# Kernel tuning notes

Measured on AMD Instinct MI355X. Metric: run time of the kernel, lower is better.

## Reference

```python
import jax, jax.numpy as jnp
import numpy as np

POOLING_COUNTS = [15, 8, 8]
N = 128
D = 256
B = 16


def _build_specs():
    # Replicates the (kernel, stride, i, j) schedule of SparseConv.__init__.
    specs = []
    stride, offset = 1, 0
    for ci, c in enumerate(POOLING_COUNTS):
        for k in range(c):
            offset += stride
            i = np.arange(0, N - offset, stride)
            j = np.arange(offset, N, stride)
            kern = 3 if (ci > 0 and k == 0) else 2  # first conv of later groups downsamples
            st = 2 if (ci > 0 and k == 0) else 1
            specs.append((kern, st, i, j))
        stride *= 2
    return specs

SPECS = _build_specs()
N_K2 = sum(1 for s in SPECS if s[0] == 2)  # 29 kernel-2 stride-1 convs
N_K3 = sum(1 for s in SPECS if s[0] == 3)  # 2 kernel-3 stride-2 convs


def _conv1d(x, w, b, stride):
    # x: (B, D, L), w: (O, I, K) -> (B, O, L_out), VALID padding like nn.Conv1d
    y = jax.lax.conv_general_dilated(x, w, (stride,), 'VALID',
                                     dimension_numbers=('NCH', 'OIH', 'NCH'))
    return y + b[None, :, None]


def setup_inputs() -> dict:
    key = jax.random.key(0)
    ks = jax.random.split(key, 5)
    scale = 1.0 / np.sqrt(2.0 * D)  # ~ PyTorch Conv1d default init scale
    return {
        'x': jax.random.normal(ks[0], (B, D, N), jnp.float32),
        'w2': jax.random.normal(ks[1], (N_K2, D, D, 2), jnp.float32) * scale,
        'b2': jax.random.normal(ks[2], (N_K2, D), jnp.float32) * scale,
        'w3': jax.random.normal(ks[3], (N_K3, D, D, 3), jnp.float32) * scale,
        'b3': jax.random.normal(ks[4], (N_K3, D), jnp.float32) * scale,
    }


def reference(x, w2, b2, w3, b3):
    diag = np.arange(N)
    # map2d[:, :, i, i] = x
    map2d = jnp.zeros((B, D, N, N), x.dtype).at[:, :, diag, diag].set(x)
    c2 = c3 = 0
    for kern, st, i, j in SPECS:  # fixed-length chain of 31 structurally distinct convs
        if kern == 2:
            x = _conv1d(x, w2[c2], b2[c2], 1)
            c2 += 1
        else:
            x = _conv1d(x, w3[c3], b3[c3], 2)
            c3 += 1
        map2d = map2d.at[:, :, i, j].set(x)  # scatter stripe into sparse 2D map
    return map2d
```

## Files before the change

kernel.cpp:

```cpp
#include <hip/hip_runtime.h>

typedef __bf16 bf16x8 __attribute__((ext_vector_type(8)));
typedef float  floatx4 __attribute__((ext_vector_type(4)));
typedef float  fvec4  __attribute__((ext_vector_type(4)));
typedef unsigned short ushort4v __attribute__((ext_vector_type(4)));
typedef unsigned short ushort8v __attribute__((ext_vector_type(8)));

__device__ __forceinline__ unsigned short f2bf(float f) {
  unsigned int u = __float_as_uint(f);
  u = u + 0x7FFFu + ((u >> 16) & 1u);
  return (unsigned short)(u >> 16);
}

#define WP3_OFF   3801088
#define X0_OFF    4194304
#define Y_OFF_B   (64u << 20)

__global__ __launch_bounds__(256) void prep_kernel(
    const float* __restrict__ w2, const float* __restrict__ w3,
    const float* __restrict__ x, unsigned short* __restrict__ ws)
{
  int g = blockIdx.x * 256 + threadIdx.x;
  const float* src; unsigned short* dst;
  if (g < 950272)            { src = w2; dst = ws; }
  else if (g < 950272+98304) { g -= 950272; src = w3; dst = ws + WP3_OFF; }
  else                       { g -= (950272+98304); src = x; dst = ws + X0_OFF; }
  fvec4 v = *reinterpret_cast<const fvec4*>(src + 4*g);
  ushort4v o;
  o[0] = f2bf(v[0]); o[1] = f2bf(v[1]); o[2] = f2bf(v[2]); o[3] = f2bf(v[3]);
  *reinterpret_cast<ushort4v*>(dst + 4*g) = o;
}

template<int KW>
__global__ __launch_bounds__(256) void conv_kernel(
    const unsigned short* __restrict__ Xin,
    unsigned short* __restrict__ Xout,
    const unsigned short* __restrict__ WP,
    const float* __restrict__ bias,
    float* __restrict__ Yl,
    int Lin, int Lpin, int Lout, int Lpout)
{
  constexpr int CS   = (KW == 3) ? 2 : 1;
  constexpr int KS   = 256 * KW;
  constexpr int pitch = KS + 8;
  constexpr int NV   = (KW == 2) ? 5 : 9;
  __shared__ unsigned short LA[32 * pitch];

  const int tid = threadIdx.x;
  const int b   = blockIdx.z;
  const int m0  = blockIdx.x * 32;
  const int n0  = blockIdx.y * 64;

  {
    const int i = tid;
    const unsigned short* rp = Xin + ((b * 256 + i) * Lpin) + CS * m0;
    ushort8v xr[NV];
#pragma unroll
    for (int v = 0; v < NV; ++v)
      xr[v] = *reinterpret_cast<const ushort8v*>(rp + v * 8);
    const unsigned short* xs = reinterpret_cast<const unsigned short*>(xr);
    if (KW == 2) {
#pragma unroll
      for (int m = 0; m < 32; ++m) {
        unsigned int pk = (unsigned int)xs[m] | ((unsigned int)xs[m + 1] << 16);
        *reinterpret_cast<unsigned int*>(&LA[m * pitch + 2 * i]) = pk;
      }
    } else {
#pragma unroll
      for (int m = 0; m < 32; ++m) {
        int base = m * pitch + 3 * i;
        LA[base]     = xs[2 * m];
        LA[base + 1] = xs[2 * m + 1];
        LA[base + 2] = xs[2 * m + 2];
      }
    }
  }
  __syncthreads();

  const int wave = tid >> 6, lane = tid & 63;
  const int l15 = lane & 15, quad = lane >> 4;
  const int nn = n0 + wave * 16 + l15;
  const unsigned short* wrow = WP + (long)nn * KS;
  const int kbase = quad * 8;

  floatx4 acc0 = {0.f, 0.f, 0.f, 0.f};
  floatx4 acc1 = {0.f, 0.f, 0.f, 0.f};

  constexpr int niter = KS / 32;
#pragma unroll
  for (int kc = 0; kc < niter; ++kc) {
    int ko = kc * 32 + kbase;
    bf16x8 bfrag = *reinterpret_cast<const bf16x8*>(wrow + ko);
    bf16x8 a0 = *reinterpret_cast<const bf16x8*>(&LA[l15 * pitch + ko]);
    bf16x8 a1 = *reinterpret_cast<const bf16x8*>(&LA[(16 + l15) * pitch + ko]);
    acc0 = __builtin_amdgcn_mfma_f32_16x16x32_bf16(a0, bfrag, acc0, 0, 0, 0);
    acc1 = __builtin_amdgcn_mfma_f32_16x16x32_bf16(a1, bfrag, acc1, 0, 0, 0);
  }

  const float bv = bias[nn];
  const int row = b * 256 + nn;
  unsigned short* xo = Xout + row * Lpout;
  float* yo = Yl + row * 128;
#pragma unroll
  for (int r = 0; r < 4; ++r) {
    int m = m0 + quad * 4 + r;
    if (m < Lout) {
      float v = acc0[r] + bv;
      xo[m] = f2bf(v);
      yo[m] = v;
    }
    int m2 = m0 + 16 + quad * 4 + r;
    if (m2 < Lout) {
      float v = acc1[r] + bv;
      xo[m2] = f2bf(v);
      yo[m2] = v;
    }
  }
}

__global__ __launch_bounds__(256) void assemble_kernel(
    float* __restrict__ out, const float* __restrict__ x, const float* __restrict__ Y)
{
  __shared__ float S[32 * 129];
  const int blk = blockIdx.x;
  const int tid = threadIdx.x;

  {
    const int m = tid & 127, half = tid >> 7;
#pragma unroll
    for (int lp = 0; lp < 16; ++lp) {
      const int l = lp * 2 + half;
      if (l < 31) {
        const int Lout = (l < 15) ? (127 - l)
                       : (l == 15) ? 56
                       : (l < 23)  ? (71 - l)
                       : (l == 23) ? 24 : (47 - l);
        if (m < Lout) S[l * 129 + m] = Y[(long)l * 524288 + blk * 128 + m];
      } else {
        S[31 * 129 + m] = x[blk * 128 + m];
      }
    }
  }
  __syncthreads();

  const long obase = (long)blk << 14;
#pragma unroll 1
  for (int it = 0; it < 16; ++it) {
    const int flat = it * 256 + tid;
    const int r = flat >> 5, c0 = (flat & 31) << 2;
    fvec4 v = {0.f, 0.f, 0.f, 0.f};
#pragma unroll
    for (int jj = 0; jj < 4; ++jj) {
      const int d = c0 + jj - r;
      if (d == 0)                 v[jj] = S[31 * 129 + r];
      else if (d >= 1 && d <= 15) v[jj] = S[(d - 1) * 129 + r];
      else if (d >= 17 && d <= 31 && (d & 1) == 1 && (r & 1) == 0)
        v[jj] = S[(15 + ((d - 17) >> 1)) * 129 + (r >> 1)];
      else if (d >= 35 && d <= 63 && (d & 3) == 3 && (r & 3) == 0)
        v[jj] = S[(23 + ((d - 35) >> 2)) * 129 + (r >> 2)];
    }
    *reinterpret_cast<fvec4*>(out + obase + 4 * flat) = v;
  }
}

extern "C" void kernel_launch(void* const* d_in, const int* in_sizes, int n_in,
                              void* d_out, int out_size, void* d_ws, size_t ws_size,
                              hipStream_t stream)
{
  const float* x  = (const float*)d_in[0];
  const float* w2 = (const float*)d_in[1];
  const float* b2 = (const float*)d_in[2];
  const float* w3 = (const float*)d_in[3];
  const float* b3 = (const float*)d_in[4];
  float* out = (float*)d_out;
  unsigned short* ws = (unsigned short*)d_ws;
  float* Y = (float*)((char*)d_ws + Y_OFF_B);

  prep_kernel<<<4608, 256, 0, stream>>>(w2, w3, x, ws);

  const int counts[3] = {15, 8, 8};
  int stride = 1, offset = 0;
  int Lin = 128, Lpin = 128;
  int c2 = 0, c3 = 0, lidx = 0;
  long xprev = X0_OFF;
  long xnext = xprev + (long)16 * 256 * 128 + 64;
  for (int ci = 0; ci < 3; ++ci) {
    for (int k = 0; k < counts[ci]; ++k) {
      offset += stride;
      int KW = (ci > 0 && k == 0) ? 3 : 2;
      int cs = (KW == 3) ? 2 : 1;
      int Lout = (Lin - KW) / cs + 1;
      int Lpout = (Lout + 7) & ~7;
      const unsigned short* WPt; const float* bt;
      if (KW == 2) { WPt = ws + (long)c2 * 131072; bt = b2 + c2 * 256; ++c2; }
      else         { WPt = ws + WP3_OFF + (long)c3 * 196608; bt = b3 + c3 * 256; ++c3; }
      dim3 grid((Lout + 31) / 32, 4, 16);
      if (KW == 2)
        conv_kernel<2><<<grid, 256, 0, stream>>>(
            ws + xprev, ws + xnext, WPt, bt, Y + (long)lidx * 524288,
            Lin, Lpin, Lout, Lpout);
      else
        conv_kernel<3><<<grid, 256, 0, stream>>>(
            ws + xprev, ws + xnext, WPt, bt, Y + (long)lidx * 524288,
            Lin, Lpin, Lout, Lpout);
      ++lidx;
      xprev = xnext;
      xnext += (long)16 * 256 * Lpout + 64;
      Lin = Lout; Lpin = Lpout;
    }
    stride *= 2;
  }

  assemble_kernel<<<4096, 256, 0, stream>>>(out, x, Y);
}
```

Measured before the change: 540.8 us.

## Fuse chains of conv layers into group kernels with halo tiles in LDS

```diff
diff --git a/kernel.cpp b/kernel.cpp
--- a/kernel.cpp
+++ b/kernel.cpp
@@ -14,6 +14,7 @@
 
 #define WP3_OFF   3801088
 #define X0_OFF    4194304
+#define TBL_OFF_B (32u << 20)
 #define Y_OFF_B   (64u << 20)
 
 __global__ __launch_bounds__(256) void prep_kernel(
@@ -31,47 +32,66 @@
   *reinterpret_cast<ushort4v*>(dst + 4*g) = o;
 }
 
-template<int KW>
-__global__ __launch_bounds__(256) void conv_kernel(
+__global__ __launch_bounds__(256) void tbl_kernel(unsigned short* __restrict__ tbl)
+{
+  const int g = blockIdx.x * 256 + threadIdx.x;
+  const int r = g >> 7, c = g & 127, d = c - r;
+  unsigned short v = 0xFFFFu;
+  if (d == 0) v = (unsigned short)(31 * 129 + r);
+  else if (d >= 1 && d <= 15) v = (unsigned short)((d - 1) * 129 + r);
+  else if (d >= 17 && d <= 31 && (d & 1) == 1 && (r & 1) == 0)
+    v = (unsigned short)((15 + ((d - 17) >> 1)) * 129 + (r >> 1));
+  else if (d >= 35 && d <= 63 && (d & 3) == 3 && (r & 3) == 0)
+    v = (unsigned short)((23 + ((d - 35) >> 2)) * 129 + (r >> 2));
+  tbl[g] = v;
+}
+
+template<int NL, int KW0, int TW, int LPIN, int LOUT0, int LPOUT, bool XOUT>
+__global__ __launch_bounds__(512, 2) void fused_group(
     const unsigned short* __restrict__ Xin,
     unsigned short* __restrict__ Xout,
-    const unsigned short* __restrict__ WP,
-    const float* __restrict__ bias,
-    float* __restrict__ Yl,
-    int Lin, int Lpin, int Lout, int Lpout)
-{
-  constexpr int CS   = (KW == 3) ? 2 : 1;
-  constexpr int KS   = 256 * KW;
-  constexpr int pitch = KS + 8;
-  constexpr int NV   = (KW == 2) ? 5 : 9;
-  __shared__ unsigned short LA[32 * pitch];
+    const unsigned short* __restrict__ W2base,
+    const unsigned short* __restrict__ W3,
+    const float* __restrict__ B2base,
+    const float* __restrict__ B3,
+    float* __restrict__ Ybase)
+{
+  constexpr int K3   = (KW0 == 3) ? 1 : 0;
+  constexpr int W0   = TW + NL - 1;
+  constexpr int R0   = ((W0 + 15) / 16) * 16;
+  constexpr int R1   = ((W0 - 1 + 15) / 16) * 16;
+  constexpr int P0   = (KW0 == 3) ? 776 : 520;
+  constexpr int LDSA = P0 * R0;
+  constexpr int LDSB = 520 * R1;
+  __shared__ unsigned short LA[LDSA + LDSB];
 
   const int tid = threadIdx.x;
-  const int b   = blockIdx.z;
-  const int m0  = blockIdx.x * 32;
-  const int n0  = blockIdx.y * 64;
+  const int g = blockIdx.x, b = blockIdx.y;
+  const int t0 = g * TW;
 
   {
-    const int i = tid;
-    const unsigned short* rp = Xin + ((b * 256 + i) * Lpin) + CS * m0;
+    const int i = tid & 255, h = tid >> 8;
+    constexpr int SPAN = (KW0 == 3) ? (2 * W0 + 1) : (W0 + 1);
+    constexpr int NV = (SPAN + 7) / 8;
+    constexpr int HR = (W0 + 1) / 2;
+    const unsigned short* rp = Xin + (b * 256 + i) * LPIN + ((KW0 == 3) ? 2 * t0 : t0);
     ushort8v xr[NV];
 #pragma unroll
-    for (int v = 0; v < NV; ++v)
-      xr[v] = *reinterpret_cast<const ushort8v*>(rp + v * 8);
+    for (int v = 0; v < NV; ++v) xr[v] = *reinterpret_cast<const ushort8v*>(rp + v * 8);
     const unsigned short* xs = reinterpret_cast<const unsigned short*>(xr);
-    if (KW == 2) {
-#pragma unroll
-      for (int m = 0; m < 32; ++m) {
-        unsigned int pk = (unsigned int)xs[m] | ((unsigned int)xs[m + 1] << 16);
-        *reinterpret_cast<unsigned int*>(&LA[m * pitch + 2 * i]) = pk;
-      }
-    } else {
-#pragma unroll
-      for (int m = 0; m < 32; ++m) {
-        int base = m * pitch + 3 * i;
-        LA[base]     = xs[2 * m];
-        LA[base + 1] = xs[2 * m + 1];
-        LA[base + 2] = xs[2 * m + 2];
+#pragma unroll
+    for (int rr = 0; rr < HR; ++rr) {
+      const int r = h * HR + rr;
+      if (r < W0) {
+        if (KW0 == 2) {
+          unsigned int pk = (unsigned int)xs[r] | ((unsigned int)xs[r + 1] << 16);
+          *reinterpret_cast<unsigned int*>(&LA[r * 520 + 2 * i]) = pk;
+        } else {
+          const int base = r * 776 + 3 * i;
+          LA[base]     = xs[2 * r];
+          LA[base + 1] = xs[2 * r + 1];
+          LA[base + 2] = xs[2 * r + 2];
+        }
       }
     }
   }
@@ -79,47 +99,84 @@
 
   const int wave = tid >> 6, lane = tid & 63;
   const int l15 = lane & 15, quad = lane >> 4;
-  const int nn = n0 + wave * 16 + l15;
-  const unsigned short* wrow = WP + (long)nn * KS;
-  const int kbase = quad * 8;
-
-  floatx4 acc0 = {0.f, 0.f, 0.f, 0.f};
-  floatx4 acc1 = {0.f, 0.f, 0.f, 0.f};
-
-  constexpr int niter = KS / 32;
-#pragma unroll
-  for (int kc = 0; kc < niter; ++kc) {
-    int ko = kc * 32 + kbase;
-    bf16x8 bfrag = *reinterpret_cast<const bf16x8*>(wrow + ko);
-    bf16x8 a0 = *reinterpret_cast<const bf16x8*>(&LA[l15 * pitch + ko]);
-    bf16x8 a1 = *reinterpret_cast<const bf16x8*>(&LA[(16 + l15) * pitch + ko]);
-    acc0 = __builtin_amdgcn_mfma_f32_16x16x32_bf16(a0, bfrag, acc0, 0, 0, 0);
-    acc1 = __builtin_amdgcn_mfma_f32_16x16x32_bf16(a1, bfrag, acc1, 0, 0, 0);
-  }
-
-  const float bv = bias[nn];
-  const int row = b * 256 + nn;
-  unsigned short* xo = Xout + row * Lpout;
-  float* yo = Yl + row * 128;
-#pragma unroll
-  for (int r = 0; r < 4; ++r) {
-    int m = m0 + quad * 4 + r;
-    if (m < Lout) {
-      float v = acc0[r] + bv;
-      xo[m] = f2bf(v);
-      yo[m] = v;
-    }
-    int m2 = m0 + 16 + quad * 4 + r;
-    if (m2 < Lout) {
-      float v = acc1[r] + bv;
-      xo[m2] = f2bf(v);
-      yo[m2] = v;
-    }
+  const int nA = wave * 32 + l15, nB = nA + 16;
+
+#pragma unroll 1
+  for (int j = 0; j < NL; ++j) {
+    const int  Wj   = TW + NL - 1 - j;
+    const int  MTH  = (Wj + 15) >> 4;
+    const bool isK3 = (KW0 == 3) && (j == 0);
+    const int  K    = isK3 ? 768 : 512;
+    const int  NIT  = isK3 ? 24 : 16;
+    const int  pit  = isK3 ? 776 : 520;
+    const unsigned short* Wl = isK3 ? W3 : (W2base + (long)(j - K3) * 131072);
+    const float* bl = isK3 ? B3 : (B2base + (j - K3) * 256);
+    const unsigned short* src = LA + ((j & 1) ? LDSA : 0);
+    unsigned short*       dst = LA + ((j & 1) ? 0 : LDSA);
+
+    const unsigned short* wA = Wl + nA * K + quad * 8;
+    const unsigned short* wB = Wl + nB * K + quad * 8;
+    int ab[3];
+#pragma unroll
+    for (int t = 0; t < 3; ++t) ab[t] = (t * 16 + l15) * pit + quad * 8;
+
+    floatx4 acc[2][3];
+#pragma unroll
+    for (int p = 0; p < 2; ++p)
+#pragma unroll
+      for (int t = 0; t < 3; ++t) acc[p][t] = (floatx4){0.f, 0.f, 0.f, 0.f};
+
+#pragma unroll 4
+    for (int kc = 0; kc < NIT; ++kc) {
+      bf16x8 bA = *reinterpret_cast<const bf16x8*>(wA + kc * 32);
+      bf16x8 bB = *reinterpret_cast<const bf16x8*>(wB + kc * 32);
+#pragma unroll
+      for (int t = 0; t < 3; ++t) {
+        if (t < MTH) {
+          bf16x8 a = *reinterpret_cast<const bf16x8*>(&src[ab[t] + kc * 32]);
+          acc[0][t] = __builtin_amdgcn_mfma_f32_16x16x32_bf16(a, bA, acc[0][t], 0, 0, 0);
+          acc[1][t] = __builtin_amdgcn_mfma_f32_16x16x32_bf16(a, bB, acc[1][t], 0, 0, 0);
+        }
+      }
+    }
+
+    const float bvA = bl[nA], bvB = bl[nB];
+    const int Wn = Wj - 1;
+    const int Lout = LOUT0 - j;
+#pragma unroll
+    for (int p = 0; p < 2; ++p) {
+      const int n = p ? nB : nA;
+      const float bv = p ? bvB : bvA;
+      float* yr = Ybase + (long)j * 524288 + (b * 256 + n) * 128;
+      unsigned short* xo = XOUT ? (Xout + (b * 256 + n) * LPOUT) : (unsigned short*)0;
+#pragma unroll
+      for (int t = 0; t < 3; ++t) {
+        if (t < MTH) {
+#pragma unroll
+          for (int r = 0; r < 4; ++r) {
+            const int ro = t * 16 + quad * 4 + r;
+            const float v = acc[p][t][r] + bv;
+            const unsigned short bf = f2bf(v);
+            if (j < NL - 1) {
+              if (ro < Wn)            dst[ro * 520 + 2 * n]       = bf;
+              if (ro >= 1 && ro <= Wn) dst[(ro - 1) * 520 + 2 * n + 1] = bf;
+            }
+            const int m = t0 + ro;
+            if (ro < Wj && m < Lout) {
+              yr[m] = v;
+              if (XOUT && j == NL - 1) xo[m] = bf;
+            }
+          }
+        }
+      }
+    }
+    __syncthreads();
   }
 }
 
 __global__ __launch_bounds__(256) void assemble_kernel(
-    float* __restrict__ out, const float* __restrict__ x, const float* __restrict__ Y)
+    float* __restrict__ out, const float* __restrict__ x,
+    const unsigned short* __restrict__ tbl, const float* __restrict__ Y)
 {
   __shared__ float S[32 * 129];
   const int blk = blockIdx.x;
@@ -147,17 +204,14 @@
 #pragma unroll 1
   for (int it = 0; it < 16; ++it) {
     const int flat = it * 256 + tid;
-    const int r = flat >> 5, c0 = (flat & 31) << 2;
-    fvec4 v = {0.f, 0.f, 0.f, 0.f};
+    ushort4v t4 = *reinterpret_cast<const ushort4v*>(tbl + 4 * flat);
+    fvec4 v;
 #pragma unroll
     for (int jj = 0; jj < 4; ++jj) {
-      const int d = c0 + jj - r;
-      if (d == 0)                 v[jj] = S[31 * 129 + r];
-      else if (d >= 1 && d <= 15) v[jj] = S[(d - 1) * 129 + r];
-      else if (d >= 17 && d <= 31 && (d & 1) == 1 && (r & 1) == 0)
-        v[jj] = S[(15 + ((d - 17) >> 1)) * 129 + (r >> 1)];
-      else if (d >= 35 && d <= 63 && (d & 3) == 3 && (r & 3) == 0)
-        v[jj] = S[(23 + ((d - 35) >> 2)) * 129 + (r >> 2)];
+      const unsigned short t = t4[jj];
+      const int idx = (t == 0xFFFFu) ? 0 : (int)t;
+      const float sv = S[idx];
+      v[jj] = (t == 0xFFFFu) ? 0.f : sv;
     }
     *reinterpret_cast<fvec4*>(out + obase + 4 * flat) = v;
   }
@@ -174,42 +228,28 @@
   const float* b3 = (const float*)d_in[4];
   float* out = (float*)d_out;
   unsigned short* ws = (unsigned short*)d_ws;
+  unsigned short* tbl = (unsigned short*)((char*)d_ws + TBL_OFF_B);
   float* Y = (float*)((char*)d_ws + Y_OFF_B);
 
+  unsigned short* X0 = ws + X0_OFF;
+  unsigned short* X1 = X0 + 524288 + 64;
+  unsigned short* X2 = X1 + 491520 + 64;
+  unsigned short* X3 = X2 + 491520 + 64;
+
   prep_kernel<<<4608, 256, 0, stream>>>(w2, w3, x, ws);
-
-  const int counts[3] = {15, 8, 8};
-  int stride = 1, offset = 0;
-  int Lin = 128, Lpin = 128;
-  int c2 = 0, c3 = 0, lidx = 0;
-  long xprev = X0_OFF;
-  long xnext = xprev + (long)16 * 256 * 128 + 64;
-  for (int ci = 0; ci < 3; ++ci) {
-    for (int k = 0; k < counts[ci]; ++k) {
-      offset += stride;
-      int KW = (ci > 0 && k == 0) ? 3 : 2;
-      int cs = (KW == 3) ? 2 : 1;
-      int Lout = (Lin - KW) / cs + 1;
-      int Lpout = (Lout + 7) & ~7;
-      const unsigned short* WPt; const float* bt;
-      if (KW == 2) { WPt = ws + (long)c2 * 131072; bt = b2 + c2 * 256; ++c2; }
-      else         { WPt = ws + WP3_OFF + (long)c3 * 196608; bt = b3 + c3 * 256; ++c3; }
-      dim3 grid((Lout + 31) / 32, 4, 16);
-      if (KW == 2)
-        conv_kernel<2><<<grid, 256, 0, stream>>>(
-            ws + xprev, ws + xnext, WPt, bt, Y + (long)lidx * 524288,
-            Lin, Lpin, Lout, Lpout);
-      else
-        conv_kernel<3><<<grid, 256, 0, stream>>>(
-            ws + xprev, ws + xnext, WPt, bt, Y + (long)lidx * 524288,
-            Lin, Lpin, Lout, Lpout);
-      ++lidx;
-      xprev = xnext;
-      xnext += (long)16 * 256 * Lpout + 64;
-      Lin = Lout; Lpin = Lpout;
-    }
-    stride *= 2;
-  }
-
-  assemble_kernel<<<4096, 256, 0, stream>>>(out, x, Y);
-}
+  tbl_kernel<<<64, 256, 0, stream>>>(tbl);
+
+  fused_group<8, 2, 32, 128, 127, 120, true><<<dim3(4, 16), 512, 0, stream>>>(
+      X0, X1, ws, (const unsigned short*)0, b2, (const float*)0, Y);
+  fused_group<7, 2, 32, 120, 119, 120, true><<<dim3(4, 16), 512, 0, stream>>>(
+      X1, X2, ws + (long)8 * 131072, (const unsigned short*)0,
+      b2 + 8 * 256, (const float*)0, Y + (long)8 * 524288);
+  fused_group<8, 3, 32, 120, 56, 56, true><<<dim3(2, 16), 512, 0, stream>>>(
+      X2, X3, ws + (long)15 * 131072, ws + WP3_OFF,
+      b2 + 15 * 256, b3, Y + (long)15 * 524288);
+  fused_group<8, 3, 17, 56, 24, 56, false><<<dim3(1, 16), 512, 0, stream>>>(
+      X3, (unsigned short*)0, ws + (long)22 * 131072, ws + WP3_OFF + 196608,
+      b2 + 22 * 256, b3 + 256, Y + (long)23 * 524288);
+
+  assemble_kernel<<<4096, 256, 0, stream>>>(out, x, tbl, Y);
+}
```

After: 725.3 us. +34.1%, slower.

## Compose consecutive conv pairs into single wider convs to halve the serial chain

Applied to the files above, without the earlier changes.

```diff
diff --git a/kernel.cpp b/kernel.cpp
--- a/kernel.cpp
+++ b/kernel.cpp
@@ -12,52 +12,249 @@
   return (unsigned short)(u >> 16);
 }
 
-#define WP3_OFF   3801088
-#define X0_OFF    4194304
-#define Y_OFF_B   (64u << 20)
+#define WP3_OFF    3801088
+#define X0_OFF     4194304
+#define WT2_OFF_B  25165824
+#define TBL_OFF_B  33554432
+#define WD2_OFF_B  34603008
+#define WT3_OFF_B  42991616
+#define CP3_OFF_B  44040192
+#define CP5_OFF_B  50331648
+#define BEFF_OFF_B 52428800
+#define Y_OFF_B    (64u << 20)
 
 __global__ __launch_bounds__(256) void prep_kernel(
     const float* __restrict__ w2, const float* __restrict__ w3,
     const float* __restrict__ x, unsigned short* __restrict__ ws)
 {
   int g = blockIdx.x * 256 + threadIdx.x;
-  const float* src; unsigned short* dst;
-  if (g < 950272)            { src = w2; dst = ws; }
-  else if (g < 950272+98304) { g -= 950272; src = w3; dst = ws + WP3_OFF; }
-  else                       { g -= (950272+98304); src = x; dst = ws + X0_OFF; }
-  fvec4 v = *reinterpret_cast<const fvec4*>(src + 4*g);
-  ushort4v o;
-  o[0] = f2bf(v[0]); o[1] = f2bf(v[1]); o[2] = f2bf(v[2]); o[3] = f2bf(v[3]);
-  *reinterpret_cast<ushort4v*>(dst + 4*g) = o;
-}
-
-template<int KW>
-__global__ __launch_bounds__(256) void conv_kernel(
-    const unsigned short* __restrict__ Xin,
-    unsigned short* __restrict__ Xout,
-    const unsigned short* __restrict__ WP,
-    const float* __restrict__ bias,
-    float* __restrict__ Yl,
-    int Lin, int Lpin, int Lout, int Lpout)
-{
-  constexpr int CS   = (KW == 3) ? 2 : 1;
-  constexpr int KS   = 256 * KW;
-  constexpr int pitch = KS + 8;
-  constexpr int NV   = (KW == 2) ? 5 : 9;
-  __shared__ unsigned short LA[32 * pitch];
-
-  const int tid = threadIdx.x;
-  const int b   = blockIdx.z;
-  const int m0  = blockIdx.x * 32;
-  const int n0  = blockIdx.y * 64;
-
+  if (g < 1179648) {
+    const float* src; unsigned short* dst;
+    if (g < 950272)       { src = w2; dst = ws; }
+    else if (g < 1048576) { g -= 950272; src = w3; dst = ws + WP3_OFF; }
+    else                  { g -= 1048576; src = x; dst = ws + X0_OFF; }
+    fvec4 v = *reinterpret_cast<const fvec4*>(src + 4 * g);
+    ushort4v o;
+    o[0] = f2bf(v[0]); o[1] = f2bf(v[1]); o[2] = f2bf(v[2]); o[3] = f2bf(v[3]);
+    *reinterpret_cast<ushort4v*>(dst + 4 * g) = o;
+  } else {
+    const int h = g - 1179648;
+    const long f = (long)4 * h;
+    fvec4 v = *reinterpret_cast<const fvec4*>(w2 + f);
+    const int c = (int)((f >> 1) & 255);
+    const int n = (int)((f >> 9) & 255);
+    const int l = (int)(f >> 17);
+    unsigned short* wd = ws + (WD2_OFF_B / 2);
+    unsigned int p0 = (unsigned int)f2bf(v[0]) | ((unsigned int)f2bf(v[2]) << 16);
+    unsigned int p1 = (unsigned int)f2bf(v[1]) | ((unsigned int)f2bf(v[3]) << 16);
+    *reinterpret_cast<unsigned int*>(wd + ((l * 2 + 0) * 256 + n) * 256 + c) = p0;
+    *reinterpret_cast<unsigned int*>(wd + ((l * 2 + 1) * 256 + n) * 256 + c) = p1;
+  }
+}
+
+__global__ __launch_bounds__(256) void wt_kernel(
+    const float* __restrict__ w2, const float* __restrict__ w3,
+    unsigned short* __restrict__ ws)
+{
+  __shared__ unsigned short T[3 * 64 * 65];
+  unsigned short* wt2 = ws + WT2_OFF_B / 2;
+  unsigned short* wt3 = ws + WT3_OFF_B / 2;
+  const int bid = blockIdx.x, tid = threadIdx.x;
+  if (bid < 464) {
+    const int l = bid >> 4, t16 = bid & 15, it = t16 & 3, ct = t16 >> 2;
+    const int cc = tid >> 2, q = tid & 3;
+    const int c = ct * 64 + cc;
+    const long rb = ((long)(l * 256 + c) * 256 + it * 64 + q * 16) * 2;
+#pragma unroll
+    for (int u2 = 0; u2 < 8; ++u2) {
+      fvec4 v = *reinterpret_cast<const fvec4*>(w2 + rb + u2 * 4);
+      const int il = q * 16 + u2 * 2;
+      T[0 * 4160 + cc * 65 + il]     = f2bf(v[0]);
+      T[1 * 4160 + cc * 65 + il]     = f2bf(v[1]);
+      T[0 * 4160 + cc * 65 + il + 1] = f2bf(v[2]);
+      T[1 * 4160 + cc * 65 + il + 1] = f2bf(v[3]);
+    }
+    __syncthreads();
+    const int b = tid >> 7, rest = tid & 127, i_loc = rest >> 1, half = rest & 1;
+    unsigned short* dp = wt2 + ((long)((l * 2 + b) * 256 + it * 64 + i_loc)) * 256
+                             + ct * 64 + half * 32;
+#pragma unroll
+    for (int v8 = 0; v8 < 4; ++v8) {
+      ushort8v o;
+#pragma unroll
+      for (int e = 0; e < 8; ++e) o[e] = T[b * 4160 + (half * 32 + v8 * 8 + e) * 65 + i_loc];
+      *reinterpret_cast<ushort8v*>(dp + v8 * 8) = o;
+    }
+  } else {
+    const int u = bid - 464, g = u >> 4, t16 = u & 15, it = t16 & 3, ct = t16 >> 2;
+    const int cc = tid >> 2, q = tid & 3;
+    const int c = ct * 64 + cc;
+    const long rb = ((long)(g * 256 + c) * 256 + it * 64 + q * 16) * 3;
+#pragma unroll
+    for (int u4 = 0; u4 < 4; ++u4) {
+      fvec4 v0 = *reinterpret_cast<const fvec4*>(w3 + rb + u4 * 12);
+      fvec4 v1 = *reinterpret_cast<const fvec4*>(w3 + rb + u4 * 12 + 4);
+      fvec4 v2 = *reinterpret_cast<const fvec4*>(w3 + rb + u4 * 12 + 8);
+      const int il = q * 16 + u4 * 4;
+      float e[12] = {v0[0],v0[1],v0[2],v0[3],v1[0],v1[1],v1[2],v1[3],v2[0],v2[1],v2[2],v2[3]};
+#pragma unroll
+      for (int di = 0; di < 4; ++di)
+#pragma unroll
+        for (int tp = 0; tp < 3; ++tp)
+          T[tp * 4160 + cc * 65 + il + di] = f2bf(e[di * 3 + tp]);
+    }
+    __syncthreads();
+    if (tid < 192) {
+      const int tp = tid >> 6, i_loc = tid & 63;
+      unsigned short* dp = wt3 + ((long)((g * 3 + tp) * 256 + it * 64 + i_loc)) * 256 + ct * 64;
+#pragma unroll
+      for (int v8 = 0; v8 < 8; ++v8) {
+        ushort8v o;
+#pragma unroll
+        for (int e2 = 0; e2 < 8; ++e2) o[e2] = T[tp * 4160 + (v8 * 8 + e2) * 65 + i_loc];
+        *reinterpret_cast<ushort8v*>(dp + v8 * 8) = o;
+      }
+    }
+  }
+}
+
+__device__ __forceinline__ int lA_of_unit(int u) {
+  return (u < 7) ? 2 * u : (u < 10) ? 16 + 2 * (u - 7) : 23 + 2 * (u - 10);
+}
+
+__global__ __launch_bounds__(256) void beff_kernel(
+    const float* __restrict__ w2, const float* __restrict__ b2,
+    const float* __restrict__ b3, float* __restrict__ beff)
+{
+  __shared__ float sb[256];
+  const int u = blockIdx.x, n = threadIdx.x;
+  int lB; const float* bA;
+  if (u < 13) { const int lA = lA_of_unit(u); lB = lA + 1; bA = b2 + lA * 256; }
+  else        { lB = (u == 13) ? 15 : 22;     bA = b3 + (u - 13) * 256; }
+  sb[n] = bA[n];
+  __syncthreads();
+  const float* wr = w2 + ((long)(lB * 256 + n)) * 512;
+  float acc = 0.f;
+#pragma unroll 8
+  for (int c = 0; c < 256; c += 2) {
+    fvec4 v = *reinterpret_cast<const fvec4*>(wr + 2 * c);
+    acc += (v[0] + v[1]) * sb[c] + (v[2] + v[3]) * sb[c + 1];
+  }
+  beff[u * 256 + n] = b2[lB * 256 + n] + acc;
+}
+
+__global__ __launch_bounds__(256) void compose_kernel(unsigned short* __restrict__ ws)
+{
+  const unsigned short* wt2 = ws + WT2_OFF_B / 2;
+  const unsigned short* wt3 = ws + WT3_OFF_B / 2;
+  const unsigned short* wd2 = ws + WD2_OFF_B / 2;
+  unsigned short* cp3 = ws + CP3_OFF_B / 2;
+  unsigned short* cp5 = ws + CP5_OFF_B / 2;
+  const int tid = threadIdx.x, bid = blockIdx.x;
+  const int wave = tid >> 6, lane = tid & 63, l15 = lane & 15, quad = lane >> 4;
+  if (bid < 208) {
+    const int u = bid >> 4, t16 = bid & 15, iblk = t16 & 3, nblk = t16 >> 2;
+    const int lA = lA_of_unit(u), lB = lA + 1;
+    const int n = nblk * 64 + wave * 16 + l15;
+    floatx4 acc[3][4];
+#pragma unroll
+    for (int k = 0; k < 3; ++k)
+#pragma unroll
+      for (int t = 0; t < 4; ++t) acc[k][t] = (floatx4){0.f, 0.f, 0.f, 0.f};
+#pragma unroll
+    for (int a = 0; a < 2; ++a) {
+      const unsigned short* bp = wd2 + ((long)((lB * 2 + a) * 256 + n)) * 256 + quad * 8;
+#pragma unroll
+      for (int bb = 0; bb < 2; ++bb) {
+        const int k = a + bb;
+        const unsigned short* ap = wt2 + ((long)((lA * 2 + bb) * 256 + iblk * 64 + l15)) * 256 + quad * 8;
+#pragma unroll
+        for (int kc = 0; kc < 8; ++kc) {
+          bf16x8 bf = *reinterpret_cast<const bf16x8*>(bp + kc * 32);
+#pragma unroll
+          for (int t = 0; t < 4; ++t) {
+            bf16x8 af = *reinterpret_cast<const bf16x8*>(ap + t * 4096 + kc * 32);
+            acc[k][t] = __builtin_amdgcn_mfma_f32_16x16x32_bf16(af, bf, acc[k][t], 0, 0, 0);
+          }
+        }
+      }
+    }
+#pragma unroll
+    for (int t = 0; t < 4; ++t)
+#pragma unroll
+      for (int r = 0; r < 4; ++r) {
+        const int i = iblk * 64 + t * 16 + quad * 4 + r;
+        unsigned short* op = cp3 + ((long)(u * 256 + n)) * 768 + i * 3;
+        op[0] = f2bf(acc[0][t][r]); op[1] = f2bf(acc[1][t][r]); op[2] = f2bf(acc[2][t][r]);
+      }
+  } else {
+    const int b2i = bid - 208, v = b2i >> 5, t32 = b2i & 31, iblk = t32 & 7, nblk = t32 >> 3;
+    const int lB = v ? 22 : 15, g = v;
+    const int n = nblk * 64 + wave * 16 + l15;
+    floatx4 acc[5][2];
+#pragma unroll
+    for (int k = 0; k < 5; ++k)
+#pragma unroll
+      for (int t = 0; t < 2; ++t) acc[k][t] = (floatx4){0.f, 0.f, 0.f, 0.f};
+#pragma unroll
+    for (int a = 0; a < 2; ++a) {
+      const unsigned short* bp = wd2 + ((long)((lB * 2 + a) * 256 + n)) * 256 + quad * 8;
+#pragma unroll
+      for (int t3 = 0; t3 < 3; ++t3) {
+        const int tau = 2 * a + t3;
+        const unsigned short* ap = wt3 + ((long)((g * 3 + t3) * 256 + iblk * 32 + l15)) * 256 + quad * 8;
+#pragma unroll
+        for (int kc = 0; kc < 8; ++kc) {
+          bf16x8 bf = *reinterpret_cast<const bf16x8*>(bp + kc * 32);
+#pragma unroll
+          for (int t = 0; t < 2; ++t) {
+            bf16x8 af = *reinterpret_cast<const bf16x8*>(ap + t * 4096 + kc * 32);
+            acc[tau][t] = __builtin_amdgcn_mfma_f32_16x16x32_bf16(af, bf, acc[tau][t], 0, 0, 0);
+          }
+        }
+      }
+    }
+#pragma unroll
+    for (int t = 0; t < 2; ++t)
+#pragma unroll
+      for (int r = 0; r < 4; ++r) {
+        const int i = iblk * 32 + t * 16 + quad * 4 + r;
+        unsigned short* op = cp5 + ((long)(v * 256 + n)) * 1280 + i * 5;
+#pragma unroll
+        for (int k = 0; k < 5; ++k) op[k] = f2bf(acc[k][t][r]);
+      }
+  }
+}
+
+__global__ __launch_bounds__(256) void tbl_kernel(unsigned short* __restrict__ tbl)
+{
+  const int g = blockIdx.x * 256 + threadIdx.x;
+  const int r = g >> 7, c = g & 127, d = c - r;
+  unsigned short v = 0xFFFFu;
+  if (d == 0) v = (unsigned short)(31 * 129 + r);
+  else if (d >= 1 && d <= 15) v = (unsigned short)((d - 1) * 129 + r);
+  else if (d >= 17 && d <= 31 && (d & 1) == 1 && (r & 1) == 0)
+    v = (unsigned short)((15 + ((d - 17) >> 1)) * 129 + (r >> 1));
+  else if (d >= 35 && d <= 63 && (d & 3) == 3 && (r & 3) == 0)
+    v = (unsigned short)((23 + ((d - 35) >> 2)) * 129 + (r >> 2));
+  tbl[g] = v;
+}
+
+template<int KW, int CS>
+__device__ __forceinline__ void conv_sub(
+    const unsigned short* __restrict__ Xin, unsigned short* __restrict__ Xout,
+    const unsigned short* __restrict__ WP, const float* __restrict__ bias,
+    float* __restrict__ Yl, unsigned short* LA,
+    int Lpin, int Lout, int Lpout, int b, int m0, int n0, int tid, bool writeX)
+{
+  constexpr int KS = 256 * KW, pitch = KS + 8;
+  constexpr int NV = (CS * 31 + KW + 7) / 8;
   {
     const int i = tid;
     const unsigned short* rp = Xin + ((b * 256 + i) * Lpin) + CS * m0;
     ushort8v xr[NV];
 #pragma unroll
-    for (int v = 0; v < NV; ++v)
-      xr[v] = *reinterpret_cast<const ushort8v*>(rp + v * 8);
+    for (int v = 0; v < NV; ++v) xr[v] = *reinterpret_cast<const ushort8v*>(rp + v * 8);
     const unsigned short* xs = reinterpret_cast<const unsigned short*>(xr);
     if (KW == 2) {
 #pragma unroll
@@ -67,36 +264,26 @@
       }
     } else {
 #pragma unroll
-      for (int m = 0; m < 32; ++m) {
-        int base = m * pitch + 3 * i;
-        LA[base]     = xs[2 * m];
-        LA[base + 1] = xs[2 * m + 1];
-        LA[base + 2] = xs[2 * m + 2];
-      }
+      for (int m = 0; m < 32; ++m)
+#pragma unroll
+        for (int kk = 0; kk < KW; ++kk)
+          LA[m * pitch + KW * i + kk] = xs[CS * m + kk];
     }
   }
   __syncthreads();
-
-  const int wave = tid >> 6, lane = tid & 63;
-  const int l15 = lane & 15, quad = lane >> 4;
+  const int wave = tid >> 6, lane = tid & 63, l15 = lane & 15, quad = lane >> 4;
   const int nn = n0 + wave * 16 + l15;
-  const unsigned short* wrow = WP + (long)nn * KS;
-  const int kbase = quad * 8;
-
+  const unsigned short* wrow = WP + (long)nn * KS + quad * 8;
   floatx4 acc0 = {0.f, 0.f, 0.f, 0.f};
   floatx4 acc1 = {0.f, 0.f, 0.f, 0.f};
-
-  constexpr int niter = KS / 32;
-#pragma unroll
-  for (int kc = 0; kc < niter; ++kc) {
-    int ko = kc * 32 + kbase;
-    bf16x8 bfrag = *reinterpret_cast<const bf16x8*>(wrow + ko);
-    bf16x8 a0 = *reinterpret_cast<const bf16x8*>(&LA[l15 * pitch + ko]);
-    bf16x8 a1 = *reinterpret_cast<const bf16x8*>(&LA[(16 + l15) * pitch + ko]);
+#pragma unroll
+  for (int kc = 0; kc < KS / 32; ++kc) {
+    bf16x8 bfrag = *reinterpret_cast<const bf16x8*>(wrow + kc * 32);
+    bf16x8 a0 = *reinterpret_cast<const bf16x8*>(&LA[l15 * pitch + quad * 8 + kc * 32]);
+    bf16x8 a1 = *reinterpret_cast<const bf16x8*>(&LA[(16 + l15) * pitch + quad * 8 + kc * 32]);
     acc0 = __builtin_amdgcn_mfma_f32_16x16x32_bf16(a0, bfrag, acc0, 0, 0, 0);
     acc1 = __builtin_amdgcn_mfma_f32_16x16x32_bf16(a1, bfrag, acc1, 0, 0, 0);
   }
-
   const float bv = bias[nn];
   const int row = b * 256 + nn;
   unsigned short* xo = Xout + row * Lpout;
@@ -104,27 +291,48 @@
 #pragma unroll
   for (int r = 0; r < 4; ++r) {
     int m = m0 + quad * 4 + r;
-    if (m < Lout) {
-      float v = acc0[r] + bv;
-      xo[m] = f2bf(v);
-      yo[m] = v;
-    }
+    if (m < Lout) { float v = acc0[r] + bv; yo[m] = v; if (writeX) xo[m] = f2bf(v); }
     int m2 = m0 + 16 + quad * 4 + r;
-    if (m2 < Lout) {
-      float v = acc1[r] + bv;
-      xo[m2] = f2bf(v);
-      yo[m2] = v;
-    }
-  }
+    if (m2 < Lout) { float v = acc1[r] + bv; yo[m2] = v; if (writeX) xo[m2] = f2bf(v); }
+  }
+}
+
+template<int KWA, int KWB, int CS>
+__global__ __launch_bounds__(256) void pair_kernel(
+    const unsigned short* __restrict__ Xin, unsigned short* __restrict__ Xout,
+    const unsigned short* __restrict__ WA, const unsigned short* __restrict__ WB,
+    const float* __restrict__ biasA, const float* __restrict__ biasB,
+    float* __restrict__ YA, float* __restrict__ YB,
+    int Lpin, int LoutA, int LoutB, int Lpout)
+{
+  __shared__ unsigned short LA[32 * (256 * KWB + 8)];
+  const int tid = threadIdx.x, b = blockIdx.z, m0 = blockIdx.x * 32;
+  const int ysub = blockIdx.y >> 2, n0 = (blockIdx.y & 3) * 64;
+  if (ysub == 0)
+    conv_sub<KWA, CS>(Xin, (unsigned short*)0, WA, biasA, YA, LA,
+                      Lpin, LoutA, 0, b, m0, n0, tid, false);
+  else
+    conv_sub<KWB, CS>(Xin, Xout, WB, biasB, YB, LA,
+                      Lpin, LoutB, Lpout, b, m0, n0, tid, true);
+}
+
+__global__ __launch_bounds__(256) void single_kernel(
+    const unsigned short* __restrict__ Xin, unsigned short* __restrict__ Xout,
+    const unsigned short* __restrict__ WP, const float* __restrict__ bias,
+    float* __restrict__ Yl, int Lpin, int Lout, int Lpout)
+{
+  __shared__ unsigned short LA[32 * 520];
+  conv_sub<2, 1>(Xin, Xout, WP, bias, Yl, LA, Lpin, Lout, Lpout,
+                 blockIdx.z, blockIdx.x * 32, blockIdx.y * 64, threadIdx.x, true);
 }
 
 __global__ __launch_bounds__(256) void assemble_kernel(
-    float* __restrict__ out, const float* __restrict__ x, const float* __restrict__ Y)
+    float* __restrict__ out, const float* __restrict__ x,
+    const unsigned short* __restrict__ tbl, const float* __restrict__ Y)
 {
   __shared__ float S[32 * 129];
   const int blk = blockIdx.x;
   const int tid = threadIdx.x;
-
   {
     const int m = tid & 127, half = tid >> 7;
 #pragma unroll
@@ -142,22 +350,18 @@
     }
   }
   __syncthreads();
-
   const long obase = (long)blk << 14;
 #pragma unroll 1
   for (int it = 0; it < 16; ++it) {
     const int flat = it * 256 + tid;
-    const int r = flat >> 5, c0 = (flat & 31) << 2;
-    fvec4 v = {0.f, 0.f, 0.f, 0.f};
+    ushort4v t4 = *reinterpret_cast<const ushort4v*>(tbl + 4 * flat);
+    fvec4 v;
 #pragma unroll
     for (int jj = 0; jj < 4; ++jj) {
-      const int d = c0 + jj - r;
-      if (d == 0)                 v[jj] = S[31 * 129 + r];
-      else if (d >= 1 && d <= 15) v[jj] = S[(d - 1) * 129 + r];
-      else if (d >= 17 && d <= 31 && (d & 1) == 1 && (r & 1) == 0)
-        v[jj] = S[(15 + ((d - 17) >> 1)) * 129 + (r >> 1)];
-      else if (d >= 35 && d <= 63 && (d & 3) == 3 && (r & 3) == 0)
-        v[jj] = S[(23 + ((d - 35) >> 2)) * 129 + (r >> 2)];
+      const unsigned short t = t4[jj];
+      const int idx = (t == 0xFFFFu) ? 0 : (int)t;
+      const float sv = S[idx];
+      v[jj] = (t == 0xFFFFu) ? 0.f : sv;
     }
     *reinterpret_cast<fvec4*>(out + obase + 4 * flat) = v;
   }
@@ -174,42 +378,88 @@
   const float* b3 = (const float*)d_in[4];
   float* out = (float*)d_out;
   unsigned short* ws = (unsigned short*)d_ws;
+  unsigned short* tbl = (unsigned short*)((char*)d_ws + TBL_OFF_B);
+  unsigned short* cp3 = ws + CP3_OFF_B / 2;
+  unsigned short* cp5 = ws + CP5_OFF_B / 2;
+  float* beff = (float*)((char*)d_ws + BEFF_OFF_B);
   float* Y = (float*)((char*)d_ws + Y_OFF_B);
-
-  prep_kernel<<<4608, 256, 0, stream>>>(w2, w3, x, ws);
-
-  const int counts[3] = {15, 8, 8};
-  int stride = 1, offset = 0;
-  int Lin = 128, Lpin = 128;
-  int c2 = 0, c3 = 0, lidx = 0;
-  long xprev = X0_OFF;
-  long xnext = xprev + (long)16 * 256 * 128 + 64;
-  for (int ci = 0; ci < 3; ++ci) {
-    for (int k = 0; k < counts[ci]; ++k) {
-      offset += stride;
-      int KW = (ci > 0 && k == 0) ? 3 : 2;
-      int cs = (KW == 3) ? 2 : 1;
-      int Lout = (Lin - KW) / cs + 1;
-      int Lpout = (Lout + 7) & ~7;
-      const unsigned short* WPt; const float* bt;
-      if (KW == 2) { WPt = ws + (long)c2 * 131072; bt = b2 + c2 * 256; ++c2; }
-      else         { WPt = ws + WP3_OFF + (long)c3 * 196608; bt = b3 + c3 * 256; ++c3; }
-      dim3 grid((Lout + 31) / 32, 4, 16);
-      if (KW == 2)
-        conv_kernel<2><<<grid, 256, 0, stream>>>(
-            ws + xprev, ws + xnext, WPt, bt, Y + (long)lidx * 524288,
-            Lin, Lpin, Lout, Lpout);
-      else
-        conv_kernel<3><<<grid, 256, 0, stream>>>(
-            ws + xprev, ws + xnext, WPt, bt, Y + (long)lidx * 524288,
-            Lin, Lpin, Lout, Lpout);
-      ++lidx;
-      xprev = xnext;
-      xnext += (long)16 * 256 * Lpout + 64;
-      Lin = Lout; Lpin = Lpout;
-    }
-    stride *= 2;
-  }
-
-  assemble_kernel<<<4096, 256, 0, stream>>>(out, x, Y);
-}
+  unsigned short* wp2 = ws;
+  unsigned short* wp3 = ws + WP3_OFF;
+
+  prep_kernel<<<8320, 256, 0, stream>>>(w2, w3, x, ws);
+  wt_kernel<<<496, 256, 0, stream>>>(w2, w3, ws);
+  tbl_kernel<<<64, 256, 0, stream>>>(tbl);
+  beff_kernel<<<15, 256, 0, stream>>>(w2, b2, b3, beff);
+  compose_kernel<<<272, 256, 0, stream>>>(ws);
+
+  long xcur = X0_OFF; int Pcur = 128, Lcur = 128;
+  long xnext = xcur + 524288 + 64;
+
+  for (int s = 0; s < 7; ++s) {
+    const int jA = 2 * s;
+    const int LoutA = Lcur - 1, LoutB = Lcur - 2;
+    const int Pout = (LoutB + 7) & ~7;
+    dim3 grid((LoutA + 31) / 32, 8, 16);
+    pair_kernel<2, 3, 1><<<grid, 256, 0, stream>>>(
+        ws + xcur, ws + xnext, wp2 + (long)jA * 131072, cp3 + (long)s * 196608,
+        b2 + jA * 256, beff + s * 256,
+        Y + (long)jA * 524288, Y + (long)(jA + 1) * 524288,
+        Pcur, LoutA, LoutB, Pout);
+    xcur = xnext; xnext += (long)16 * 256 * Pout + 64; Pcur = Pout; Lcur = LoutB;
+  }
+  {
+    const int Lout = Lcur - 1, Pout = (Lout + 7) & ~7;
+    single_kernel<<<dim3((Lout + 31) / 32, 4, 16), 256, 0, stream>>>(
+        ws + xcur, ws + xnext, wp2 + (long)14 * 131072, b2 + 14 * 256,
+        Y + (long)14 * 524288, Pcur, Lout, Pout);
+    xcur = xnext; xnext += (long)16 * 256 * Pout + 64; Pcur = Pout; Lcur = Lout;
+  }
+  {
+    const int LoutA = (Lcur - 3) / 2 + 1, LoutB = LoutA - 1;
+    const int Pout = (LoutB + 7) & ~7;
+    dim3 grid((LoutA + 31) / 32, 8, 16);
+    pair_kernel<3, 5, 2><<<grid, 256, 0, stream>>>(
+        ws + xcur, ws + xnext, wp3, cp5,
+        b3, beff + 13 * 256,
+        Y + (long)15 * 524288, Y + (long)16 * 524288,
+        Pcur, LoutA, LoutB, Pout);
+    xcur = xnext; xnext += (long)16 * 256 * Pout + 64; Pcur = Pout; Lcur = LoutB;
+  }
+  for (int s = 0; s < 3; ++s) {
+    const int jA = 17 + 2 * s, w2i = 16 + 2 * s, unit = 7 + s;
+    const int LoutA = Lcur - 1, LoutB = Lcur - 2;
+    const int Pout = (LoutB + 7) & ~7;
+    dim3 grid((LoutA + 31) / 32, 8, 16);
+    pair_kernel<2, 3, 1><<<grid, 256, 0, stream>>>(
+        ws + xcur, ws + xnext, wp2 + (long)w2i * 131072, cp3 + (long)unit * 196608,
+        b2 + w2i * 256, beff + unit * 256,
+        Y + (long)jA * 524288, Y + (long)(jA + 1) * 524288,
+        Pcur, LoutA, LoutB, Pout);
+    xcur = xnext; xnext += (long)16 * 256 * Pout + 64; Pcur = Pout; Lcur = LoutB;
+  }
+  {
+    const int LoutA = (Lcur - 3) / 2 + 1, LoutB = LoutA - 1;
+    const int Pout = (LoutB + 7) & ~7;
+    dim3 grid((LoutA + 31) / 32, 8, 16);
+    pair_kernel<3, 5, 2><<<grid, 256, 0, stream>>>(
+        ws + xcur, ws + xnext, wp3 + 196608, cp5 + 327680,
+        b3 + 256, beff + 14 * 256,
+        Y + (long)23 * 524288, Y + (long)24 * 524288,
+        Pcur, LoutA, LoutB, Pout);
+    xcur = xnext; xnext += (long)16 * 256 * Pout + 64; Pcur = Pout; Lcur = LoutB;
+  }
+  for (int s = 0; s < 3; ++s) {
+    const int jA = 25 + 2 * s, w2i = 23 + 2 * s, unit = 10 + s;
+    const int LoutA = Lcur - 1, LoutB = Lcur - 2;
+    const int Pout = (LoutB + 7) & ~7;
+    dim3 grid((LoutA + 31) / 32, 8, 16);
+    pair_kernel<2, 3, 1><<<grid, 256, 0, stream>>>(
+        ws + xcur, ws + xnext, wp2 + (long)w2i * 131072, cp3 + (long)unit * 196608,
+        b2 + w2i * 256, beff + unit * 256,
+        Y + (long)jA * 524288, Y + (long)(jA + 1) * 524288,
+        Pcur, LoutA, LoutB, Pout);
+    xcur = xnext; xnext += (long)16 * 256 * Pout + 64; Pcur = Pout; Lcur = LoutB;
+  }
+
+  assemble_kernel<<<4096, 256, 0, stream>>>(out, x, tbl, Y);
+}
```

Result: slower. 579.8 us (+7.2%).

## Halve conv M-tile for more blocks and table-drive the 2D map assembly

Applied to the files above, without the earlier changes.

```diff
diff --git a/kernel.cpp b/kernel.cpp
--- a/kernel.cpp
+++ b/kernel.cpp
@@ -14,6 +14,7 @@
 
 #define WP3_OFF   3801088
 #define X0_OFF    4194304
+#define TBL_E     16777216
 #define Y_OFF_B   (64u << 20)
 
 __global__ __launch_bounds__(256) void prep_kernel(
@@ -31,6 +32,21 @@
   *reinterpret_cast<ushort4v*>(dst + 4*g) = o;
 }
 
+__global__ __launch_bounds__(256) void tbl_kernel(unsigned short* __restrict__ tbl)
+{
+  const int g = blockIdx.x * 256 + threadIdx.x;
+  const int h = g >> 13, rl = (g >> 7) & 63, c = g & 127;
+  const int r = h * 64 + rl, d = c - r;
+  unsigned short v = 0xFFFFu;
+  if (d == 0) v = (unsigned short)(31 * 65 + rl);
+  else if (d >= 1 && d <= 15) v = (unsigned short)((d - 1) * 65 + rl);
+  else if (d >= 17 && d <= 31 && (d & 1) == 1 && (r & 1) == 0)
+    v = (unsigned short)((15 + ((d - 17) >> 1)) * 65 + (rl >> 1));
+  else if (d >= 35 && d <= 63 && (d & 3) == 3 && (r & 3) == 0)
+    v = (unsigned short)((23 + ((d - 35) >> 2)) * 65 + (rl >> 2));
+  tbl[g] = v;
+}
+
 template<int KW>
 __global__ __launch_bounds__(256) void conv_kernel(
     const unsigned short* __restrict__ Xin,
@@ -38,17 +54,18 @@
     const unsigned short* __restrict__ WP,
     const float* __restrict__ bias,
     float* __restrict__ Yl,
-    int Lin, int Lpin, int Lout, int Lpout)
-{
-  constexpr int CS   = (KW == 3) ? 2 : 1;
-  constexpr int KS   = 256 * KW;
+    int Lpin, int Lout, int Lpout)
+{
+  constexpr int CS    = (KW == 3) ? 2 : 1;
+  constexpr int KS    = 256 * KW;
   constexpr int pitch = KS + 8;
-  constexpr int NV   = (KW == 2) ? 5 : 9;
-  __shared__ unsigned short LA[32 * pitch];
+  constexpr int SPAN  = CS * 15 + KW;
+  constexpr int NV    = (SPAN + 7) / 8;
+  __shared__ unsigned short LA[16 * pitch];
 
   const int tid = threadIdx.x;
   const int b   = blockIdx.z;
-  const int m0  = blockIdx.x * 32;
+  const int m0  = blockIdx.x * 16;
   const int n0  = blockIdx.y * 64;
 
   {
@@ -61,13 +78,13 @@
     const unsigned short* xs = reinterpret_cast<const unsigned short*>(xr);
     if (KW == 2) {
 #pragma unroll
-      for (int m = 0; m < 32; ++m) {
+      for (int m = 0; m < 16; ++m) {
         unsigned int pk = (unsigned int)xs[m] | ((unsigned int)xs[m + 1] << 16);
         *reinterpret_cast<unsigned int*>(&LA[m * pitch + 2 * i]) = pk;
       }
     } else {
 #pragma unroll
-      for (int m = 0; m < 32; ++m) {
+      for (int m = 0; m < 16; ++m) {
         int base = m * pitch + 3 * i;
         LA[base]     = xs[2 * m];
         LA[base + 1] = xs[2 * m + 1];
@@ -80,84 +97,84 @@
   const int wave = tid >> 6, lane = tid & 63;
   const int l15 = lane & 15, quad = lane >> 4;
   const int nn = n0 + wave * 16 + l15;
-  const unsigned short* wrow = WP + (long)nn * KS;
-  const int kbase = quad * 8;
-
-  floatx4 acc0 = {0.f, 0.f, 0.f, 0.f};
-  floatx4 acc1 = {0.f, 0.f, 0.f, 0.f};
-
+  const float bv = bias[nn];
+  const unsigned short* wrow = WP + (long)nn * KS + quad * 8;
+
+  floatx4 acc = {0.f, 0.f, 0.f, 0.f};
   constexpr int niter = KS / 32;
 #pragma unroll
   for (int kc = 0; kc < niter; ++kc) {
-    int ko = kc * 32 + kbase;
-    bf16x8 bfrag = *reinterpret_cast<const bf16x8*>(wrow + ko);
-    bf16x8 a0 = *reinterpret_cast<const bf16x8*>(&LA[l15 * pitch + ko]);
-    bf16x8 a1 = *reinterpret_cast<const bf16x8*>(&LA[(16 + l15) * pitch + ko]);
-    acc0 = __builtin_amdgcn_mfma_f32_16x16x32_bf16(a0, bfrag, acc0, 0, 0, 0);
-    acc1 = __builtin_amdgcn_mfma_f32_16x16x32_bf16(a1, bfrag, acc1, 0, 0, 0);
-  }
-
-  const float bv = bias[nn];
+    bf16x8 bfrag = *reinterpret_cast<const bf16x8*>(wrow + kc * 32);
+    bf16x8 a = *reinterpret_cast<const bf16x8*>(&LA[l15 * pitch + quad * 8 + kc * 32]);
+    acc = __builtin_amdgcn_mfma_f32_16x16x32_bf16(a, bfrag, acc, 0, 0, 0);
+  }
+
   const int row = b * 256 + nn;
-  unsigned short* xo = Xout + row * Lpout;
-  float* yo = Yl + row * 128;
+  unsigned short* xo = Xout + (long)row * Lpout;
+  float* yo = Yl + (long)row * 128;
 #pragma unroll
   for (int r = 0; r < 4; ++r) {
-    int m = m0 + quad * 4 + r;
+    const int m = m0 + quad * 4 + r;
     if (m < Lout) {
-      float v = acc0[r] + bv;
+      const float v = acc[r] + bv;
       xo[m] = f2bf(v);
       yo[m] = v;
     }
-    int m2 = m0 + 16 + quad * 4 + r;
-    if (m2 < Lout) {
-      float v = acc1[r] + bv;
-      xo[m2] = f2bf(v);
-      yo[m2] = v;
-    }
   }
 }
 
 __global__ __launch_bounds__(256) void assemble_kernel(
-    float* __restrict__ out, const float* __restrict__ x, const float* __restrict__ Y)
-{
-  __shared__ float S[32 * 129];
-  const int blk = blockIdx.x;
+    float* __restrict__ out, const float* __restrict__ x,
+    const unsigned short* __restrict__ tbl, const float* __restrict__ Y)
+{
+  __shared__ float S[32 * 65];
+  const int bh = blockIdx.x;
+  const int blk = bh >> 1, h = bh & 1;
   const int tid = threadIdx.x;
 
-  {
-    const int m = tid & 127, half = tid >> 7;
-#pragma unroll
-    for (int lp = 0; lp < 16; ++lp) {
-      const int l = lp * 2 + half;
-      if (l < 31) {
-        const int Lout = (l < 15) ? (127 - l)
-                       : (l == 15) ? 56
-                       : (l < 23)  ? (71 - l)
-                       : (l == 23) ? 24 : (47 - l);
-        if (m < Lout) S[l * 129 + m] = Y[(long)l * 524288 + blk * 128 + m];
-      } else {
-        S[31 * 129 + m] = x[blk * 128 + m];
-      }
+  ushort4v t4s[8];
+  const unsigned short* tb = tbl + h * 8192;
+#pragma unroll
+  for (int it = 0; it < 8; ++it)
+    t4s[it] = *reinterpret_cast<const ushort4v*>(tb + 4 * (it * 256 + tid));
+
+#pragma unroll
+  for (int p = 0; p < 8; ++p) {
+    const int idx = p * 256 + tid;
+    const int slot = idx >> 6, m = idx & 63;
+    if (slot < 15) {
+      const int mm = h * 64 + m;
+      if (mm < 127 - slot) S[slot * 65 + m] = Y[(long)slot * 524288 + blk * 128 + mm];
+    } else if (slot < 23) {
+      if (m < 32) {
+        const int mm = h * 32 + m;
+        const int Lout = (slot == 15) ? 56 : (71 - slot);
+        if (mm < Lout) S[slot * 65 + m] = Y[(long)slot * 524288 + blk * 128 + mm];
+      }
+    } else if (slot < 31) {
+      if (m < 16) {
+        const int mm = h * 16 + m;
+        const int Lout = (slot == 23) ? 24 : (47 - slot);
+        if (mm < Lout) S[slot * 65 + m] = Y[(long)slot * 524288 + blk * 128 + mm];
+      }
+    } else {
+      S[31 * 65 + m] = x[blk * 128 + h * 64 + m];
     }
   }
   __syncthreads();
 
-  const long obase = (long)blk << 14;
-#pragma unroll 1
-  for (int it = 0; it < 16; ++it) {
+  const long obase = ((long)blk << 14) + ((long)h << 13);
+#pragma unroll
+  for (int it = 0; it < 8; ++it) {
     const int flat = it * 256 + tid;
-    const int r = flat >> 5, c0 = (flat & 31) << 2;
-    fvec4 v = {0.f, 0.f, 0.f, 0.f};
+    const ushort4v t4 = t4s[it];
+    fvec4 v;
 #pragma unroll
     for (int jj = 0; jj < 4; ++jj) {
-      const int d = c0 + jj - r;
-      if (d == 0)                 v[jj] = S[31 * 129 + r];
-      else if (d >= 1 && d <= 15) v[jj] = S[(d - 1) * 129 + r];
-      else if (d >= 17 && d <= 31 && (d & 1) == 1 && (r & 1) == 0)
-        v[jj] = S[(15 + ((d - 17) >> 1)) * 129 + (r >> 1)];
-      else if (d >= 35 && d <= 63 && (d & 3) == 3 && (r & 3) == 0)
-        v[jj] = S[(23 + ((d - 35) >> 2)) * 129 + (r >> 2)];
+      const unsigned short t = t4[jj];
+      const int idx = (t == 0xFFFFu) ? 0 : (int)t;
+      const float sv = S[idx];
+      v[jj] = (t == 0xFFFFu) ? 0.f : sv;
     }
     *reinterpret_cast<fvec4*>(out + obase + 4 * flat) = v;
   }
@@ -174,9 +191,11 @@
   const float* b3 = (const float*)d_in[4];
   float* out = (float*)d_out;
   unsigned short* ws = (unsigned short*)d_ws;
+  unsigned short* tbl = ws + TBL_E;
   float* Y = (float*)((char*)d_ws + Y_OFF_B);
 
   prep_kernel<<<4608, 256, 0, stream>>>(w2, w3, x, ws);
+  tbl_kernel<<<64, 256, 0, stream>>>(tbl);
 
   const int counts[3] = {15, 8, 8};
   int stride = 1, offset = 0;
@@ -194,15 +213,15 @@
       const unsigned short* WPt; const float* bt;
       if (KW == 2) { WPt = ws + (long)c2 * 131072; bt = b2 + c2 * 256; ++c2; }
       else         { WPt = ws + WP3_OFF + (long)c3 * 196608; bt = b3 + c3 * 256; ++c3; }
-      dim3 grid((Lout + 31) / 32, 4, 16);
+      dim3 grid((Lout + 15) / 16, 4, 16);
       if (KW == 2)
         conv_kernel<2><<<grid, 256, 0, stream>>>(
             ws + xprev, ws + xnext, WPt, bt, Y + (long)lidx * 524288,
-            Lin, Lpin, Lout, Lpout);
+            Lpin, Lout, Lpout);
       else
         conv_kernel<3><<<grid, 256, 0, stream>>>(
             ws + xprev, ws + xnext, WPt, bt, Y + (long)lidx * 524288,
-            Lin, Lpin, Lout, Lpout);
+            Lpin, Lout, Lpout);
       ++lidx;
       xprev = xnext;
       xnext += (long)16 * 256 * Lpout + 64;
@@ -211,5 +230,5 @@
     stride *= 2;
   }
 
-  assemble_kernel<<<4096, 256, 0, stream>>>(out, x, Y);
-}
+  assemble_kernel<<<8192, 256, 0, stream>>>(out, x, tbl, Y);
+}
```

Result: slower. 562.3 us (+4.0%).
